# Kernel optimization log

Hardware: AMD Instinct MI355X
Metric: run time of the kernel (lower is better)

Reference implementation:

```python
import jax, jax.numpy as jnp
import numpy as np


def setup_inputs() -> dict:
    key = jax.random.key(0)
    ks = jax.random.split(key, 9)
    I, J, H, B = 1024, 1024, 32, 1024
    hid = 10
    d_in = 3 + 3 * H  # 99
    return {
        "X": jax.random.normal(ks[0], (B, I), dtype=jnp.float32),
        "weight": jax.random.normal(ks[1], (I, J), dtype=jnp.float32) * 0.1,
        "hidden_state": jax.random.normal(ks[2], (I, J, H), dtype=jnp.float32) * 0.1,
        "W1": jax.random.normal(ks[3], (d_in, hid), dtype=jnp.float32) / np.sqrt(d_in),
        "b1": jax.random.normal(ks[4], (hid,), dtype=jnp.float32) * 0.01,
        "W2": jax.random.normal(ks[5], (hid, hid), dtype=jnp.float32) / np.sqrt(hid),
        "b2": jax.random.normal(ks[6], (hid,), dtype=jnp.float32) * 0.01,
        "W3": jax.random.normal(ks[7], (hid, 1 + H), dtype=jnp.float32) / np.sqrt(hid),
        "b3": jax.random.normal(ks[8], (1 + H,), dtype=jnp.float32) * 0.01,
    }


def reference(X, weight, hidden_state, W1, b1, W2, b2, W3, b3):
    I, J = weight.shape
    H = hidden_state.shape[-1]
    # Leave-one-out means, computed once via full sums (the original recomputes
    # slice+concat+mean per cell in nested Python loops: O(I*J*(I+J)) work).
    fwd_w = (jnp.sum(weight, axis=0, keepdims=True) - weight) / (I - 1)  # (I,J) col mean excl. row i
    bwd_w = (jnp.sum(weight, axis=1, keepdims=True) - weight) / (J - 1)  # (I,J) row mean excl. col j
    fwd_h = (jnp.sum(hidden_state, axis=0, keepdims=True) - hidden_state) / (I - 1)  # (I,J,H)
    bwd_h = (jnp.sum(hidden_state, axis=1, keepdims=True) - hidden_state) / (J - 1)  # (I,J,H)
    # Per-cell feature: [w_ij, mean_fwd_w, mean_bwd_w, h_ij, mean_fwd_h, mean_bwd_h] -> (I,J,3+3H)
    feat = jnp.concatenate(
        [weight[..., None], fwd_w[..., None], bwd_w[..., None], hidden_state, fwd_h, bwd_h],
        axis=-1,
    )
    # Tiny 3-layer MLP batched over all cells (local_nn).
    h = jax.nn.relu(feat @ W1 + b1)
    h = jax.nn.relu(h @ W2 + b2)
    upd = h @ W3 + b3  # (I,J,1+H)
    new_weight = weight + upd[..., 0]
    new_hidden = hidden_state + upd[..., 1:]
    probs = jax.nn.softmax(X @ new_weight, axis=-1)  # (B,J)
    return probs, new_weight, new_hidden
```

## Files before the change

### kernel.cpp

```cpp
#include <hip/hip_runtime.h>

#define I_DIM 1024
#define J_DIM 1024
#define INV_I1 (1.0f/1023.0f)
#define INV_J1 (1.0f/1023.0f)

#define WS_CW     0
#define WS_RW     1024
#define WS_CH     2048
#define WS_PJT    34816
#define WS_QI     45056
#define WS_CST    55296
#define WS_LOGITS 65536
#define WS_RHP    65536
#define WS_WCP    327680
#define WS_HPART  344064


__global__ __launch_bounds__(512) void k_red1(const float* __restrict__ Hd,
                                              float* __restrict__ hpart,
                                              float* __restrict__ rhpart,
                                              int npart) {
  __shared__ float4 s4[512];
  int t = threadIdx.x;
  int wv = t >> 6, lane = t & 63;
  int p = blockIdx.x >> 3, c = blockIdx.x & 7;
  int R = 1024 / npart;
  int i0 = p * R;
  float4 ca0 = make_float4(0.f,0.f,0.f,0.f);
  float4 ca1 = make_float4(0.f,0.f,0.f,0.f);
  for (int g = 0; g < R; g += 8) {
    #pragma unroll
    for (int r = 0; r < 8; r++) {
      int i = i0 + g + r;
      const float4* rowc = (const float4*)(Hd + (size_t)i * 32768 + c * 4096);
      float4 v0 = rowc[t];
      float4 v1 = rowc[t + 512];
      ca0.x += v0.x; ca0.y += v0.y; ca0.z += v0.z; ca0.w += v0.w;
      ca1.x += v1.x; ca1.y += v1.y; ca1.z += v1.z; ca1.w += v1.w;
      float4 rs;
      rs.x = v0.x + v1.x; rs.y = v0.y + v1.y;
      rs.z = v0.z + v1.z; rs.w = v0.w + v1.w;
      #pragma unroll
      for (int off = 8; off <= 32; off <<= 1) {
        rs.x += __shfl_xor(rs.x, off, 64);
        rs.y += __shfl_xor(rs.y, off, 64);
        rs.z += __shfl_xor(rs.z, off, 64);
        rs.w += __shfl_xor(rs.w, off, 64);
      }
      if (lane < 8) s4[(r * 8 + wv) * 8 + lane] = rs;
    }
    __syncthreads();
    if (t < 64) {
      int r = t >> 3, ln = t & 7;
      float4 a = s4[(r * 8 + 0) * 8 + ln];
      #pragma unroll
      for (int w2 = 1; w2 < 8; w2++) {
        float4 b = s4[(r * 8 + w2) * 8 + ln];
        a.x += b.x; a.y += b.y; a.z += b.z; a.w += b.w;
      }
      int i = i0 + g + r;
      ((float4*)rhpart)[i * 64 + c * 8 + ln] = a;
    }
    __syncthreads();
  }
  float4* hp = (float4*)(hpart + (size_t)p * 32768 + c * 4096);
  hp[t] = ca0;
  hp[t + 512] = ca1;
}

__global__ __launch_bounds__(256) void k_wred(const float* __restrict__ W,
                                              float* __restrict__ ws,
                                              float* __restrict__ wcp) {
  int b = blockIdx.x, t = threadIdx.x;
  if (b < 128) {
    int wv = t >> 6, lane = t & 63;
    #pragma unroll
    for (int rr = 0; rr < 2; rr++) {
      int row = b * 8 + wv * 2 + rr;
      float acc = 0.f;
      #pragma unroll
      for (int m = 0; m < 16; m++) acc += W[row * 1024 + lane + 64 * m];
      #pragma unroll
      for (int off = 32; off > 0; off >>= 1) acc += __shfl_down(acc, off, 64);
      if (lane == 0) ws[WS_RW + row] = acc;
    }
  } else {
    int p = b - 128;
    float a0 = 0.f, a1 = 0.f, a2 = 0.f, a3 = 0.f;
    for (int i = p * 64; i < p * 64 + 64; i++) {
      const float* row = W + (size_t)i * 1024;
      a0 += row[t]; a1 += row[t + 256]; a2 += row[t + 512]; a3 += row[t + 768];
    }
    wcp[p * 1024 + t] = a0;       wcp[p * 1024 + t + 256] = a1;
    wcp[p * 1024 + t + 512] = a2; wcp[p * 1024 + t + 768] = a3;
  }
}

__global__ __launch_bounds__(256) void k_red2(const float* __restrict__ hpart,
                                              const float* __restrict__ wcp,
                                              float* __restrict__ ws, int npart) {
  int b = blockIdx.x, t = threadIdx.x;
  if (b < 128) {
    int col = b * 256 + t;
    float acc = 0.f;
    for (int p = 0; p < npart; p++) acc += hpart[(size_t)p * 32768 + col];
    ws[WS_CH + col] = acc;
  } else {
    int col = (b - 128) * 256 + t;
    float acc = 0.f;
    #pragma unroll
    for (int p = 0; p < 16; p++) acc += wcp[p * 1024 + col];
    ws[WS_CW + col] = acc;
  }
}

__global__ __launch_bounds__(256) void k_pq(const float* __restrict__ W1,
                                            const float* __restrict__ b1,
                                            const float* __restrict__ W2,
                                            const float* __restrict__ b2,
                                            const float* __restrict__ W3,
                                            const float* __restrict__ b3,
                                            float* __restrict__ ws,
                                            const float* __restrict__ rhpart) {
  if (blockIdx.x == 8) {
    int t = threadIdx.x;
    for (int idx = t; idx < 330; idx += 256) {
      int r = idx / 10, q = idx - r * 10;
      float v;
      if (r == 0)
        v = W1[q] - W1[10 + q] * INV_I1 - W1[20 + q] * INV_J1;
      else
        v = W1[(2 + r) * 10 + q] - W1[(34 + r) * 10 + q] * INV_I1 - W1[(66 + r) * 10 + q] * INV_J1;
      ws[WS_CST + idx] = v;
    }
    for (int idx = t; idx < 100; idx += 256) ws[WS_CST + 330 + idx] = W2[idx];
    for (int idx = t; idx < 330; idx += 256) {
      int o = idx / 10, q2 = idx - o * 10;
      ws[WS_CST + 430 + idx] = W3[q2 * 33 + o];
    }
    if (t < 10) ws[WS_CST + 760 + t] = b2[t];
    if (t < 33) ws[WS_CST + 770 + t] = b3[t];
    return;
  }
  int gid = blockIdx.x * 256 + threadIdx.x;
  float out[10];
  if (gid < 1024) {
    int j = gid;
    float sc = ws[WS_CW + j] * INV_I1;
    #pragma unroll
    for (int q = 0; q < 10; q++) out[q] = sc * W1[10 + q];
    for (int k = 0; k < 32; k++) {
      float cc = ws[WS_CH + j * 32 + k] * INV_I1;
      #pragma unroll
      for (int q = 0; q < 10; q++) out[q] += cc * W1[(35 + k) * 10 + q];
    }
    #pragma unroll
    for (int q = 0; q < 10; q++) ws[WS_PJT + q * 1024 + j] = out[q];
  } else {
    int i = gid - 1024;
    float rh[32];
    #pragma unroll
    for (int k = 0; k < 32; k++) rh[k] = 0.f;
    for (int c = 0; c < 8; c++) {
      #pragma unroll
      for (int k = 0; k < 32; k++) rh[k] += rhpart[i * 256 + c * 32 + k];
    }
    float sr = ws[WS_RW + i] * INV_J1;
    #pragma unroll
    for (int q = 0; q < 10; q++) out[q] = b1[q] + sr * W1[20 + q];
    for (int k = 0; k < 32; k++) {
      float cc = rh[k] * INV_J1;
      #pragma unroll
      for (int q = 0; q < 10; q++) out[q] += cc * W1[(67 + k) * 10 + q];
    }
    #pragma unroll
    for (int q = 0; q < 10; q++) ws[WS_QI + i * 10 + q] = out[q];
  }
}

__global__ __launch_bounds__(256) void k_mlp(
    const float* __restrict__ W, const float* __restrict__ Hd,
    const float* __restrict__ ws,
    float* __restrict__ newW, float* __restrict__ newH) {
  __shared__ __align__(16) float hbuf[8192];
  int t = threadIdx.x;
  int cell0 = blockIdx.x * 256;
  int i = blockIdx.x >> 2;
  int j0 = (blockIdx.x & 3) * 256;
  const float* cst = ws + WS_CST;

  const float4* src = (const float4*)(Hd + (size_t)cell0 * 32);
  #pragma unroll
  for (int m = 0; m < 8; m++) {
    int s = t + 256 * m;
    float4 v = src[s];
    int cs = s >> 3, ms = s & 7;
    int slot = cs * 8 + ((ms + cs) & 7);
    *(float4*)&hbuf[slot * 4] = v;
  }
  float w0 = W[cell0 + t];
  float pj[10];
  #pragma unroll
  for (int q = 0; q < 10; q++) pj[q] = ws[WS_PJT + q * 1024 + j0 + t];
  float qv[10];
  #pragma unroll
  for (int q = 0; q < 10; q++) qv[q] = ws[WS_QI + i * 10 + q];
  __syncthreads();

  float h[32];
  #pragma unroll
  for (int m = 0; m < 8; m++) {
    int slot = t * 8 + ((m + t) & 7);
    float4 v = *(const float4*)&hbuf[slot * 4];
    h[m * 4 + 0] = v.x; h[m * 4 + 1] = v.y; h[m * 4 + 2] = v.z; h[m * 4 + 3] = v.w;
  }

  float z[10];
  #pragma unroll
  for (int q = 0; q < 10; q++) z[q] = pj[q] + qv[q] + w0 * cst[q];
  #pragma unroll
  for (int k = 0; k < 32; k++) {
    #pragma unroll
    for (int q = 0; q < 10; q++) z[q] += h[k] * cst[(k + 1) * 10 + q];
  }
  #pragma unroll
  for (int q = 0; q < 10; q++) z[q] = fmaxf(z[q], 0.f);

  float y[10];
  #pragma unroll
  for (int q2 = 0; q2 < 10; q2++) y[q2] = cst[760 + q2];
  #pragma unroll
  for (int q = 0; q < 10; q++) {
    #pragma unroll
    for (int q2 = 0; q2 < 10; q2++) y[q2] += z[q] * cst[330 + q * 10 + q2];
  }
  #pragma unroll
  for (int q2 = 0; q2 < 10; q2++) y[q2] = fmaxf(y[q2], 0.f);

  float u = cst[770];
  #pragma unroll
  for (int q2 = 0; q2 < 10; q2++) u += y[q2] * cst[430 + q2];
  newW[cell0 + t] = w0 + u;

  #pragma unroll
  for (int o = 1; o < 33; o++) {
    float a = cst[770 + o];
    #pragma unroll
    for (int q2 = 0; q2 < 10; q2++) a += y[q2] * cst[430 + o * 10 + q2];
    h[o - 1] += a;
  }

  #pragma unroll
  for (int m = 0; m < 8; m++) {
    int slot = t * 8 + ((m + t) & 7);
    *(float4*)&hbuf[slot * 4] = make_float4(h[m * 4], h[m * 4 + 1], h[m * 4 + 2], h[m * 4 + 3]);
  }
  __syncthreads();
  float4* dst = (float4*)(newH + (size_t)cell0 * 32);
  #pragma unroll
  for (int m = 0; m < 8; m++) {
    int s = t + 256 * m;
    int cs = s >> 3, ms = s & 7;
    int slot = cs * 8 + ((ms + cs) & 7);
    dst[s] = *(const float4*)&hbuf[slot * 4];
  }
}

__global__ __launch_bounds__(256) void k_gemm(const float* __restrict__ A,
                                              const float* __restrict__ B,
                                              float* __restrict__ C) {
  __shared__ float As[16][68];
  __shared__ float Bs[16][68];
  int t = threadIdx.x;
  int bm = blockIdx.y, bn = blockIdx.x;
  int ar = t >> 2, ak = (t & 3) << 2;
  int bk = t >> 4, bnc = (t & 15) << 2;
  int tm = (t >> 4) << 2, tn = (t & 15) << 2;
  const float* Ap = A + (bm * 64 + ar) * 1024 + ak;
  const float* Bp = B + bk * 1024 + bn * 64 + bnc;
  float acc[4][4] = {};
  float4 av = *(const float4*)Ap;
  float4 bv = *(const float4*)Bp;
  for (int k0 = 0; k0 < 1024; k0 += 16) {
    __syncthreads();
    As[ak + 0][ar] = av.x; As[ak + 1][ar] = av.y;
    As[ak + 2][ar] = av.z; As[ak + 3][ar] = av.w;
    *(float4*)&Bs[bk][bnc] = bv;
    __syncthreads();
    if (k0 + 16 < 1024) {
      av = *(const float4*)(Ap + k0 + 16);
      bv = *(const float4*)(Bp + (k0 + 16) * 1024);
    }
    #pragma unroll
    for (int kk = 0; kk < 16; kk++) {
      float4 a4 = *(const float4*)&As[kk][tm];
      float4 b4 = *(const float4*)&Bs[kk][tn];
      acc[0][0] += a4.x * b4.x; acc[0][1] += a4.x * b4.y; acc[0][2] += a4.x * b4.z; acc[0][3] += a4.x * b4.w;
      acc[1][0] += a4.y * b4.x; acc[1][1] += a4.y * b4.y; acc[1][2] += a4.y * b4.z; acc[1][3] += a4.y * b4.w;
      acc[2][0] += a4.z * b4.x; acc[2][1] += a4.z * b4.y; acc[2][2] += a4.z * b4.z; acc[2][3] += a4.z * b4.w;
      acc[3][0] += a4.w * b4.x; acc[3][1] += a4.w * b4.y; acc[3][2] += a4.w * b4.z; acc[3][3] += a4.w * b4.w;
    }
  }
  #pragma unroll
  for (int r = 0; r < 4; r++) {
    *(float4*)&C[(bm * 64 + tm + r) * 1024 + bn * 64 + tn] =
        make_float4(acc[r][0], acc[r][1], acc[r][2], acc[r][3]);
  }
}

__global__ __launch_bounds__(256) void k_softmax(const float* __restrict__ L,
                                                 float* __restrict__ P) {
  __shared__ float sm[4], ss[4];
  int r = blockIdx.x, t = threadIdx.x;
  const float* row = L + r * 1024;
  float v0 = row[t], v1 = row[t + 256], v2 = row[t + 512], v3 = row[t + 768];
  float m = fmaxf(fmaxf(v0, v1), fmaxf(v2, v3));
  #pragma unroll
  for (int off = 32; off > 0; off >>= 1) m = fmaxf(m, __shfl_xor(m, off, 64));
  int wv = t >> 6, lane = t & 63;
  if (lane == 0) sm[wv] = m;
  __syncthreads();
  m = fmaxf(fmaxf(sm[0], sm[1]), fmaxf(sm[2], sm[3]));
  float e0 = expf(v0 - m), e1 = expf(v1 - m), e2 = expf(v2 - m), e3 = expf(v3 - m);
  float s = e0 + e1 + e2 + e3;
  #pragma unroll
  for (int off = 32; off > 0; off >>= 1) s += __shfl_xor(s, off, 64);
  if (lane == 0) ss[wv] = s;
  __syncthreads();
  s = ss[0] + ss[1] + ss[2] + ss[3];
  float inv = 1.0f / s;
  float* prow = P + r * 1024;
  prow[t] = e0 * inv; prow[t + 256] = e1 * inv;
  prow[t + 512] = e2 * inv; prow[t + 768] = e3 * inv;
}

extern "C" void kernel_launch(void* const* d_in, const int* in_sizes, int n_in,
                              void* d_out, int out_size, void* d_ws, size_t ws_size,
                              hipStream_t stream) {
  const float* X  = (const float*)d_in[0];
  const float* W  = (const float*)d_in[1];
  const float* Hd = (const float*)d_in[2];
  const float* W1 = (const float*)d_in[3];
  const float* b1 = (const float*)d_in[4];
  const float* W2 = (const float*)d_in[5];
  const float* b2 = (const float*)d_in[6];
  const float* W3 = (const float*)d_in[7];
  const float* b3 = (const float*)d_in[8];
  float* out   = (float*)d_out;
  float* probs = out;
  float* newW  = out + 1024 * 1024;
  float* newH  = out + 2 * 1024 * 1024;
  float* ws = (float*)d_ws;

  size_t wsf = ws_size / 4;
  int npart = 64;
  while (npart > 8 && (size_t)WS_HPART + (size_t)npart * 32768ull > wsf) npart >>= 1;
  float* rhpart = ws + WS_RHP;
  float* wcp    = ws + WS_WCP;
  float* hpart  = ws + WS_HPART;

  k_red1<<<npart * 8, 512, 0, stream>>>(Hd, hpart, rhpart, npart);
  k_wred<<<144, 256, 0, stream>>>(W, ws, wcp);
  k_red2<<<132, 256, 0, stream>>>(hpart, wcp, ws, npart);
  k_pq<<<9, 256, 0, stream>>>(W1, b1, W2, b2, W3, b3, ws, rhpart);
  k_mlp<<<4096, 256, 0, stream>>>(W, Hd, ws, newW, newH);
  k_gemm<<<dim3(16, 16), 256, 0, stream>>>(X, newW, ws + WS_LOGITS);
  k_softmax<<<1024, 256, 0, stream>>>(ws + WS_LOGITS, probs);
}
```

Measured before the change: 170.2 us.

## Use split-bf16 MFMA GEMM for logits and fuse reduction kernels

```diff
diff --git a/kernel.cpp b/kernel.cpp
--- a/kernel.cpp
+++ b/kernel.cpp
@@ -1,7 +1,5 @@
 #include <hip/hip_runtime.h>
 
-#define I_DIM 1024
-#define J_DIM 1024
 #define INV_I1 (1.0f/1023.0f)
 #define INV_J1 (1.0f/1023.0f)
 
@@ -16,6 +14,18 @@
 #define WS_WCP    327680
 #define WS_HPART  344064
 
+typedef __attribute__((ext_vector_type(8))) short bf16x8;
+typedef __attribute__((ext_vector_type(4))) float f32x4;
+
+__device__ inline ushort bf16_rne(float x) {
+  union { float f; unsigned u; } v; v.f = x;
+  unsigned r = v.u + 0x7fffu + ((v.u >> 16) & 1u);
+  return (ushort)(r >> 16);
+}
+__device__ inline float bf16_tof(ushort h) {
+  union { unsigned u; float f; } c; c.u = ((unsigned)h) << 16;
+  return c.f;
+}
 
 __global__ __launch_bounds__(512) void k_red1(const float* __restrict__ Hd,
                                               float* __restrict__ hpart,
@@ -70,8 +80,10 @@
 }
 
 __global__ __launch_bounds__(256) void k_wred(const float* __restrict__ W,
+                                              const float* __restrict__ X,
                                               float* __restrict__ ws,
-                                              float* __restrict__ wcp) {
+                                              float* __restrict__ wcp,
+                                              ushort* __restrict__ Xb) {
   int b = blockIdx.x, t = threadIdx.x;
   if (b < 128) {
     int wv = t >> 6, lane = t & 63;
@@ -85,7 +97,7 @@
       for (int off = 32; off > 0; off >>= 1) acc += __shfl_down(acc, off, 64);
       if (lane == 0) ws[WS_RW + row] = acc;
     }
-  } else {
+  } else if (b < 144) {
     int p = b - 128;
     float a0 = 0.f, a1 = 0.f, a2 = 0.f, a3 = 0.f;
     for (int i = p * 64; i < p * 64 + 64; i++) {
@@ -94,37 +106,79 @@
     }
     wcp[p * 1024 + t] = a0;       wcp[p * 1024 + t + 256] = a1;
     wcp[p * 1024 + t + 512] = a2; wcp[p * 1024 + t + 768] = a3;
-  }
-}
-
-__global__ __launch_bounds__(256) void k_red2(const float* __restrict__ hpart,
-                                              const float* __restrict__ wcp,
-                                              float* __restrict__ ws, int npart) {
+  } else {
+    int g = (b - 144) * 256 + t;
+    float4 v0 = ((const float4*)X)[g * 2];
+    float4 v1 = ((const float4*)X)[g * 2 + 1];
+    float xs[8] = {v0.x, v0.y, v0.z, v0.w, v1.x, v1.y, v1.z, v1.w};
+    ushort hi[8], lo[8];
+    #pragma unroll
+    for (int e = 0; e < 8; e++) {
+      hi[e] = bf16_rne(xs[e]);
+      lo[e] = bf16_rne(xs[e] - bf16_tof(hi[e]));
+    }
+    ((uint4*)Xb)[g] = *(uint4*)hi;
+    ((uint4*)(Xb + 1048576))[g] = *(uint4*)lo;
+  }
+}
+
+__global__ __launch_bounds__(256) void k_red2pq(const float* __restrict__ hpart,
+                                                const float* __restrict__ wcp,
+                                                const float* __restrict__ rhpart,
+                                                const float* __restrict__ W1,
+                                                const float* __restrict__ b1,
+                                                const float* __restrict__ W2,
+                                                const float* __restrict__ b2,
+                                                const float* __restrict__ W3,
+                                                const float* __restrict__ b3,
+                                                float* __restrict__ ws, int npart) {
   int b = blockIdx.x, t = threadIdx.x;
   if (b < 128) {
+    __shared__ float chl[256];
+    __shared__ float cwl[8];
     int col = b * 256 + t;
     float acc = 0.f;
     for (int p = 0; p < npart; p++) acc += hpart[(size_t)p * 32768 + col];
     ws[WS_CH + col] = acc;
+    chl[t] = acc;
+    if (t < 8) {
+      int j = b * 8 + t;
+      float a = 0.f;
+      #pragma unroll
+      for (int p = 0; p < 16; p++) a += wcp[p * 1024 + j];
+      ws[WS_CW + j] = a;
+      cwl[t] = a;
+    }
+    __syncthreads();
+    if (t < 80) {
+      int jj = t / 10, q = t - jj * 10;
+      int j = b * 8 + jj;
+      float o = cwl[jj] * INV_I1 * W1[10 + q];
+      for (int k = 0; k < 32; k++)
+        o += chl[jj * 32 + k] * INV_I1 * W1[(35 + k) * 10 + q];
+      ws[WS_PJT + q * 1024 + j] = o;
+    }
+  } else if (b < 132) {
+    int i = (b - 128) * 256 + t;
+    float rh[32];
+    #pragma unroll
+    for (int k = 0; k < 32; k++) rh[k] = 0.f;
+    for (int c = 0; c < 8; c++) {
+      #pragma unroll
+      for (int k = 0; k < 32; k++) rh[k] += rhpart[i * 256 + c * 32 + k];
+    }
+    float sr = ws[WS_RW + i] * INV_J1;
+    float out[10];
+    #pragma unroll
+    for (int q = 0; q < 10; q++) out[q] = b1[q] + sr * W1[20 + q];
+    for (int k = 0; k < 32; k++) {
+      float cc = rh[k] * INV_J1;
+      #pragma unroll
+      for (int q = 0; q < 10; q++) out[q] += cc * W1[(67 + k) * 10 + q];
+    }
+    #pragma unroll
+    for (int q = 0; q < 10; q++) ws[WS_QI + i * 10 + q] = out[q];
   } else {
-    int col = (b - 128) * 256 + t;
-    float acc = 0.f;
-    #pragma unroll
-    for (int p = 0; p < 16; p++) acc += wcp[p * 1024 + col];
-    ws[WS_CW + col] = acc;
-  }
-}
-
-__global__ __launch_bounds__(256) void k_pq(const float* __restrict__ W1,
-                                            const float* __restrict__ b1,
-                                            const float* __restrict__ W2,
-                                            const float* __restrict__ b2,
-                                            const float* __restrict__ W3,
-                                            const float* __restrict__ b3,
-                                            float* __restrict__ ws,
-                                            const float* __restrict__ rhpart) {
-  if (blockIdx.x == 8) {
-    int t = threadIdx.x;
     for (int idx = t; idx < 330; idx += 256) {
       int r = idx / 10, q = idx - r * 10;
       float v;
@@ -141,41 +195,6 @@
     }
     if (t < 10) ws[WS_CST + 760 + t] = b2[t];
     if (t < 33) ws[WS_CST + 770 + t] = b3[t];
-    return;
-  }
-  int gid = blockIdx.x * 256 + threadIdx.x;
-  float out[10];
-  if (gid < 1024) {
-    int j = gid;
-    float sc = ws[WS_CW + j] * INV_I1;
-    #pragma unroll
-    for (int q = 0; q < 10; q++) out[q] = sc * W1[10 + q];
-    for (int k = 0; k < 32; k++) {
-      float cc = ws[WS_CH + j * 32 + k] * INV_I1;
-      #pragma unroll
-      for (int q = 0; q < 10; q++) out[q] += cc * W1[(35 + k) * 10 + q];
-    }
-    #pragma unroll
-    for (int q = 0; q < 10; q++) ws[WS_PJT + q * 1024 + j] = out[q];
-  } else {
-    int i = gid - 1024;
-    float rh[32];
-    #pragma unroll
-    for (int k = 0; k < 32; k++) rh[k] = 0.f;
-    for (int c = 0; c < 8; c++) {
-      #pragma unroll
-      for (int k = 0; k < 32; k++) rh[k] += rhpart[i * 256 + c * 32 + k];
-    }
-    float sr = ws[WS_RW + i] * INV_J1;
-    #pragma unroll
-    for (int q = 0; q < 10; q++) out[q] = b1[q] + sr * W1[20 + q];
-    for (int k = 0; k < 32; k++) {
-      float cc = rh[k] * INV_J1;
-      #pragma unroll
-      for (int q = 0; q < 10; q++) out[q] += cc * W1[(67 + k) * 10 + q];
-    }
-    #pragma unroll
-    for (int q = 0; q < 10; q++) ws[WS_QI + i * 10 + q] = out[q];
   }
 }
 
@@ -267,45 +286,86 @@
   }
 }
 
-__global__ __launch_bounds__(256) void k_gemm(const float* __restrict__ A,
-                                              const float* __restrict__ B,
+__global__ __launch_bounds__(256) void k_wt(const float* __restrict__ nW,
+                                            ushort* __restrict__ Wt) {
+  __shared__ float buf[64][65];
+  int t = threadIdx.x;
+  int i0 = blockIdx.y * 64, j0 = blockIdx.x * 64;
+  int jl = t & 63, rr = t >> 6;
+  #pragma unroll
+  for (int r2 = 0; r2 < 16; r2++) {
+    int il = r2 * 4 + rr;
+    buf[jl][il] = nW[(size_t)(i0 + il) * 1024 + j0 + jl];
+  }
+  __syncthreads();
+  int jw = t >> 2, iq = (t & 3) * 16;
+  ushort hi[16], lo[16];
+  #pragma unroll
+  for (int e = 0; e < 16; e++) {
+    float x = buf[jw][iq + e];
+    ushort h = bf16_rne(x);
+    hi[e] = h;
+    lo[e] = bf16_rne(x - bf16_tof(h));
+  }
+  size_t base = (size_t)(j0 + jw) * 1024 + i0 + iq;
+  *(uint4*)(Wt + base)     = *(uint4*)hi;
+  *(uint4*)(Wt + base + 8) = *(uint4*)(hi + 8);
+  *(uint4*)(Wt + 1048576 + base)     = *(uint4*)lo;
+  *(uint4*)(Wt + 1048576 + base + 8) = *(uint4*)(lo + 8);
+}
+
+__global__ __launch_bounds__(256) void k_gemm(const ushort* __restrict__ Xb,
+                                              const ushort* __restrict__ Wt,
                                               float* __restrict__ C) {
-  __shared__ float As[16][68];
-  __shared__ float Bs[16][68];
   int t = threadIdx.x;
-  int bm = blockIdx.y, bn = blockIdx.x;
-  int ar = t >> 2, ak = (t & 3) << 2;
-  int bk = t >> 4, bnc = (t & 15) << 2;
-  int tm = (t >> 4) << 2, tn = (t & 15) << 2;
-  const float* Ap = A + (bm * 64 + ar) * 1024 + ak;
-  const float* Bp = B + bk * 1024 + bn * 64 + bnc;
-  float acc[4][4] = {};
-  float4 av = *(const float4*)Ap;
-  float4 bv = *(const float4*)Bp;
-  for (int k0 = 0; k0 < 1024; k0 += 16) {
-    __syncthreads();
-    As[ak + 0][ar] = av.x; As[ak + 1][ar] = av.y;
-    As[ak + 2][ar] = av.z; As[ak + 3][ar] = av.w;
-    *(float4*)&Bs[bk][bnc] = bv;
-    __syncthreads();
-    if (k0 + 16 < 1024) {
-      av = *(const float4*)(Ap + k0 + 16);
-      bv = *(const float4*)(Bp + (k0 + 16) * 1024);
-    }
-    #pragma unroll
-    for (int kk = 0; kk < 16; kk++) {
-      float4 a4 = *(const float4*)&As[kk][tm];
-      float4 b4 = *(const float4*)&Bs[kk][tn];
-      acc[0][0] += a4.x * b4.x; acc[0][1] += a4.x * b4.y; acc[0][2] += a4.x * b4.z; acc[0][3] += a4.x * b4.w;
-      acc[1][0] += a4.y * b4.x; acc[1][1] += a4.y * b4.y; acc[1][2] += a4.y * b4.z; acc[1][3] += a4.y * b4.w;
-      acc[2][0] += a4.z * b4.x; acc[2][1] += a4.z * b4.y; acc[2][2] += a4.z * b4.z; acc[2][3] += a4.z * b4.w;
-      acc[3][0] += a4.w * b4.x; acc[3][1] += a4.w * b4.y; acc[3][2] += a4.w * b4.z; acc[3][3] += a4.w * b4.w;
-    }
-  }
+  int w = t >> 6, l = t & 63;
+  int m0 = blockIdx.y * 64 + (w >> 1) * 32;
+  int n0 = blockIdx.x * 64 + (w & 1) * 32;
+  int lr = l & 15;
+  int kg = (l >> 4) * 8;
+  const ushort* Xhi = Xb;
+  const ushort* Xlo = Xb + 1048576;
+  const ushort* Whi = Wt;
+  const ushort* Wlo = Wt + 1048576;
+  const size_t ra0 = (size_t)(m0 + lr) * 1024;
+  const size_t ra1 = (size_t)(m0 + 16 + lr) * 1024;
+  const size_t cb0 = (size_t)(n0 + lr) * 1024;
+  const size_t cb1 = (size_t)(n0 + 16 + lr) * 1024;
+  f32x4 acc00 = {0.f, 0.f, 0.f, 0.f};
+  f32x4 acc01 = {0.f, 0.f, 0.f, 0.f};
+  f32x4 acc10 = {0.f, 0.f, 0.f, 0.f};
+  f32x4 acc11 = {0.f, 0.f, 0.f, 0.f};
+  #pragma unroll 2
+  for (int k0 = 0; k0 < 1024; k0 += 32) {
+    int o = k0 + kg;
+    bf16x8 ah0 = *(const bf16x8*)(Xhi + ra0 + o);
+    bf16x8 ah1 = *(const bf16x8*)(Xhi + ra1 + o);
+    bf16x8 al0 = *(const bf16x8*)(Xlo + ra0 + o);
+    bf16x8 al1 = *(const bf16x8*)(Xlo + ra1 + o);
+    bf16x8 bh0 = *(const bf16x8*)(Whi + cb0 + o);
+    bf16x8 bh1 = *(const bf16x8*)(Whi + cb1 + o);
+    bf16x8 bl0 = *(const bf16x8*)(Wlo + cb0 + o);
+    bf16x8 bl1 = *(const bf16x8*)(Wlo + cb1 + o);
+    acc00 = __builtin_amdgcn_mfma_f32_16x16x32_bf16(ah0, bh0, acc00, 0, 0, 0);
+    acc01 = __builtin_amdgcn_mfma_f32_16x16x32_bf16(ah0, bh1, acc01, 0, 0, 0);
+    acc10 = __builtin_amdgcn_mfma_f32_16x16x32_bf16(ah1, bh0, acc10, 0, 0, 0);
+    acc11 = __builtin_amdgcn_mfma_f32_16x16x32_bf16(ah1, bh1, acc11, 0, 0, 0);
+    acc00 = __builtin_amdgcn_mfma_f32_16x16x32_bf16(ah0, bl0, acc00, 0, 0, 0);
+    acc01 = __builtin_amdgcn_mfma_f32_16x16x32_bf16(ah0, bl1, acc01, 0, 0, 0);
+    acc10 = __builtin_amdgcn_mfma_f32_16x16x32_bf16(ah1, bl0, acc10, 0, 0, 0);
+    acc11 = __builtin_amdgcn_mfma_f32_16x16x32_bf16(ah1, bl1, acc11, 0, 0, 0);
+    acc00 = __builtin_amdgcn_mfma_f32_16x16x32_bf16(al0, bh0, acc00, 0, 0, 0);
+    acc01 = __builtin_amdgcn_mfma_f32_16x16x32_bf16(al0, bh1, acc01, 0, 0, 0);
+    acc10 = __builtin_amdgcn_mfma_f32_16x16x32_bf16(al1, bh0, acc10, 0, 0, 0);
+    acc11 = __builtin_amdgcn_mfma_f32_16x16x32_bf16(al1, bh1, acc11, 0, 0, 0);
+  }
+  int rbase = m0 + (l >> 4) * 4;
   #pragma unroll
   for (int r = 0; r < 4; r++) {
-    *(float4*)&C[(bm * 64 + tm + r) * 1024 + bn * 64 + tn] =
-        make_float4(acc[r][0], acc[r][1], acc[r][2], acc[r][3]);
+    C[(size_t)(rbase + r) * 1024 + n0 + lr]           = acc00[r];
+    C[(size_t)(rbase + r) * 1024 + n0 + 16 + lr]      = acc01[r];
+    C[(size_t)(rbase + 16 + r) * 1024 + n0 + lr]      = acc10[r];
+    C[(size_t)(rbase + 16 + r) * 1024 + n0 + 16 + lr] = acc11[r];
   }
 }
 
@@ -355,16 +415,22 @@
 
   size_t wsf = ws_size / 4;
   int npart = 64;
-  while (npart > 8 && (size_t)WS_HPART + (size_t)npart * 32768ull > wsf) npart >>= 1;
-  float* rhpart = ws + WS_RHP;
-  float* wcp    = ws + WS_WCP;
-  float* hpart  = ws + WS_HPART;
+  while (npart > 8 &&
+         (size_t)WS_HPART + (size_t)npart * 32768ull + 2097152ull > wsf)
+    npart >>= 1;
+  float*  rhpart = ws + WS_RHP;
+  float*  wcp    = ws + WS_WCP;
+  float*  hpart  = ws + WS_HPART;
+  size_t  xb0    = (size_t)WS_HPART + (size_t)npart * 32768ull;
+  ushort* Xb     = (ushort*)(ws + xb0);
+  ushort* Wt     = (ushort*)(ws + xb0 + 1048576);
 
   k_red1<<<npart * 8, 512, 0, stream>>>(Hd, hpart, rhpart, npart);
-  k_wred<<<144, 256, 0, stream>>>(W, ws, wcp);
-  k_red2<<<132, 256, 0, stream>>>(hpart, wcp, ws, npart);
-  k_pq<<<9, 256, 0, stream>>>(W1, b1, W2, b2, W3, b3, ws, rhpart);
+  k_wred<<<656, 256, 0, stream>>>(W, X, ws, wcp, Xb);
+  k_red2pq<<<133, 256, 0, stream>>>(hpart, wcp, rhpart, W1, b1, W2, b2, W3, b3,
+                                    ws, npart);
   k_mlp<<<4096, 256, 0, stream>>>(W, Hd, ws, newW, newH);
-  k_gemm<<<dim3(16, 16), 256, 0, stream>>>(X, newW, ws + WS_LOGITS);
+  k_wt<<<dim3(16, 16), 256, 0, stream>>>(newW, Wt);
+  k_gemm<<<dim3(16, 16), 256, 0, stream>>>(Xb, Wt, ws + WS_LOGITS);
   k_softmax<<<1024, 256, 0, stream>>>(ws + WS_LOGITS, probs);
 }
```

Result: faster. 157.1 us (-7.7%).
